# Optimization experiments

Measured on AMD Instinct MI355X. Metric: run time of the kernel, lower is better.

The kernel has to match this reference:

```python
import jax, jax.numpy as jnp
import numpy as np

DIM = 512
HEADS = 8
HEAD_DIM = DIM // HEADS
MLP_HIDDEN = int(DIM * 4.0)
B, N = 4, 2048
LS_INIT = 1e-5
EPS = 1e-5


def _layernorm(x, w, b):
    mu = jnp.mean(x, axis=-1, keepdims=True)
    var = jnp.mean(jnp.square(x - mu), axis=-1, keepdims=True)
    return (x - mu) * jax.lax.rsqrt(var + EPS) * w + b


def setup_inputs() -> dict:
    key = jax.random.key(0)
    ks = jax.random.split(key, 12)
    s = 0.02
    return {
        "x": jax.random.normal(ks[0], (B, N, DIM), jnp.float32),
        "rel_pos_bias": jax.random.normal(ks[1], (HEADS, N, N), jnp.float32),
        "qkv_w": jax.random.normal(ks[2], (DIM, 3 * DIM), jnp.float32) * s,
        "qkv_b": jnp.zeros((3 * DIM,), jnp.float32),
        "out_w": jax.random.normal(ks[3], (DIM, DIM), jnp.float32) * s,
        "out_b": jnp.zeros((DIM,), jnp.float32),
        "ln1_w": jnp.ones((DIM,), jnp.float32),
        "ln1_b": jnp.zeros((DIM,), jnp.float32),
        "ln2_w": jnp.ones((DIM,), jnp.float32),
        "ln2_b": jnp.zeros((DIM,), jnp.float32),
        "ffn_w1": jax.random.normal(ks[4], (DIM, MLP_HIDDEN), jnp.float32) * s,
        "ffn_b1": jnp.zeros((MLP_HIDDEN,), jnp.float32),
        "ffn_w2": jax.random.normal(ks[5], (MLP_HIDDEN, DIM), jnp.float32) * s,
        "ffn_b2": jnp.zeros((DIM,), jnp.float32),
        "gamma1": jnp.full((DIM,), LS_INIT, jnp.float32),
        "gamma2": jnp.full((DIM,), LS_INIT, jnp.float32),
    }


def reference(x, rel_pos_bias, qkv_w, qkv_b, out_w, out_b, ln1_w, ln1_b,
              ln2_w, ln2_b, ffn_w1, ffn_b1, ffn_w2, ffn_b2, gamma1, gamma2):
    # Pre-norm MHA with relative-position bias
    y = _layernorm(x, ln1_w, ln1_b)                       # [B,N,C]
    qkv = y @ qkv_w + qkv_b                               # [B,N,3C]
    qkv = qkv.reshape(B, N, 3, HEADS, HEAD_DIM)
    q = jnp.transpose(qkv[:, :, 0], (0, 2, 1, 3))         # [B,H,N,D]
    k = jnp.transpose(qkv[:, :, 1], (0, 2, 1, 3))
    v = jnp.transpose(qkv[:, :, 2], (0, 2, 1, 3))
    scale = 1.0 / np.sqrt(HEAD_DIM).astype(np.float32)
    attn = jnp.einsum("bhid,bhjd->bhij", q, k) * scale    # [B,H,N,N]
    attn = attn + rel_pos_bias[None]
    attn = jax.nn.softmax(attn, axis=-1)
    out = jnp.einsum("bhij,bhjd->bhid", attn, v)          # [B,H,N,D]
    out = jnp.transpose(out, (0, 2, 1, 3)).reshape(B, N, DIM)
    out = out @ out_w + out_b
    x = x + out * gamma1                                  # layer scale, no drop-path (eval)
    # FFN with exact GELU
    y2 = _layernorm(x, ln2_w, ln2_b)
    h = jax.nn.gelu(y2 @ ffn_w1 + ffn_b1, approximate=False)
    ffn_out = h @ ffn_w2 + ffn_b2
    x = x + ffn_out * gamma2
    return x
```

## Files before the change

kernel.cpp:

```cpp
#include <hip/hip_runtime.h>
#include <hip/hip_bf16.h>
#include <math.h>

#define SEQ 2048
#define BATCH 4
#define DM 512
#define NH 8
#define HD 64
#define HID 2048
#define ROWS (BATCH * SEQ)

typedef __attribute__((ext_vector_type(8))) short short8;
typedef __attribute__((ext_vector_type(4))) float f32x4;

__device__ __forceinline__ short f2bf(float f) {
    unsigned u = __float_as_uint(f);
    u += 0x7fff + ((u >> 16) & 1);
    return (short)(u >> 16);
}

__device__ __forceinline__ void gl2lds16(const void* g, void* l) {
    __builtin_amdgcn_global_load_lds(
        (const __attribute__((address_space(1))) void*)g,
        (__attribute__((address_space(3))) void*)l, 16, 0, 0);
}

__global__ __launch_bounds__(256) void tcast_all(
    const float* __restrict__ qkv_w, const float* __restrict__ out_w,
    const float* __restrict__ w1, const float* __restrict__ w2,
    short* __restrict__ o_qkv, short* __restrict__ o_out,
    short* __restrict__ o_w1, short* __restrict__ o_w2) {
    __shared__ float tile[32][33];
    int id = blockIdx.x;
    const float* W; short* O; int K, N;
    if (id < 768)       { W = qkv_w; O = o_qkv; K = 512;  N = 1536; }
    else if (id < 1024) { W = out_w; O = o_out; K = 512;  N = 512;  id -= 768; }
    else if (id < 2048) { W = w1;    O = o_w1;  K = 512;  N = 2048; id -= 1024; }
    else                { W = w2;    O = o_w2;  K = 2048; N = 512;  id -= 2048; }
    int tn = N / 32;
    int n0 = (id % tn) * 32, k0 = (id / tn) * 32;
    int tx = threadIdx.x, ty = threadIdx.y;
#pragma unroll
    for (int i = 0; i < 4; ++i)
        tile[ty + i * 8][tx] = W[(size_t)(k0 + ty + i * 8) * N + n0 + tx];
    __syncthreads();
#pragma unroll
    for (int i = 0; i < 4; ++i)
        O[(size_t)(n0 + ty + i * 8) * K + k0 + tx] = f2bf(tile[tx][ty + i * 8]);
}

__global__ __launch_bounds__(256) void ln_k(const float* __restrict__ X,
                                            const float* __restrict__ g,
                                            const float* __restrict__ bta,
                                            short* __restrict__ Y) {
    int t = threadIdx.x;
    int wv = t >> 6, ln = t & 63;
    size_t row = (size_t)blockIdx.x * 4 + wv;
    const float* xr = X + row * DM;
    float4 v0 = *(const float4*)(xr + ln * 4);
    float4 v1 = *(const float4*)(xr + 256 + ln * 4);
    float s = v0.x + v0.y + v0.z + v0.w + v1.x + v1.y + v1.z + v1.w;
    float q = v0.x * v0.x + v0.y * v0.y + v0.z * v0.z + v0.w * v0.w +
              v1.x * v1.x + v1.y * v1.y + v1.z * v1.z + v1.w * v1.w;
#pragma unroll
    for (int off = 1; off < 64; off <<= 1) {
        s += __shfl_xor(s, off);
        q += __shfl_xor(q, off);
    }
    float mean = s * (1.0f / 512.0f);
    float var = q * (1.0f / 512.0f) - mean * mean;
    float rstd = rsqrtf(var + 1e-5f);
    int c0 = ln * 4, c1 = 256 + ln * 4;
    ushort4 o0, o1;
    o0.x = (unsigned short)f2bf((v0.x - mean) * rstd * g[c0 + 0] + bta[c0 + 0]);
    o0.y = (unsigned short)f2bf((v0.y - mean) * rstd * g[c0 + 1] + bta[c0 + 1]);
    o0.z = (unsigned short)f2bf((v0.z - mean) * rstd * g[c0 + 2] + bta[c0 + 2]);
    o0.w = (unsigned short)f2bf((v0.w - mean) * rstd * g[c0 + 3] + bta[c0 + 3]);
    o1.x = (unsigned short)f2bf((v1.x - mean) * rstd * g[c1 + 0] + bta[c1 + 0]);
    o1.y = (unsigned short)f2bf((v1.y - mean) * rstd * g[c1 + 1] + bta[c1 + 1]);
    o1.z = (unsigned short)f2bf((v1.z - mean) * rstd * g[c1 + 2] + bta[c1 + 2]);
    o1.w = (unsigned short)f2bf((v1.w - mean) * rstd * g[c1 + 3] + bta[c1 + 3]);
    *(ushort4*)((unsigned short*)Y + row * DM + c0) = o0;
    *(ushort4*)((unsigned short*)Y + row * DM + c1) = o1;
}

template <int EPI, int TN>
__global__ __launch_bounds__(256) void gemm_bt(const short* __restrict__ A,
                                               const short* __restrict__ Bt,
                                               const float* __restrict__ bias,
                                               const float* __restrict__ gamma,
                                               const float* __restrict__ res,
                                               void* __restrict__ Cout,
                                               int M, int N, int K, int gx) {
    constexpr int NI = TN / 32;
    __shared__ __attribute__((aligned(16))) short As[2][2][128][32];
    __shared__ __attribute__((aligned(16))) short Bs[2][2][TN][32];
    int t = threadIdx.x;
    int w = t >> 6, ln = t & 63;
    int quad = ln >> 4, l15 = ln & 15;
    int nwg = gridDim.x;
    int qq = nwg >> 3;
    int sw = ((blockIdx.x & 7) * qq) + (blockIdx.x >> 3);
    int bx = sw % gx, by = sw / gx;
    int n0 = bx * TN, m0 = by * 128;
    int wm = (w & 1) * 64, wn = (w >> 1) * (TN / 2);

    int srow0 = w * 32 + (ln >> 2);
    int srow1 = srow0 + 16;
    int srowB = w * 16 + (ln >> 2);
    int schunk = (ln & 3) * 8;
    const short* Ag0 = A + (size_t)(m0 + srow0) * K + schunk;
    const short* Ag1 = A + (size_t)(m0 + srow1) * K + schunk;
    const short* Bg0 = Bt + (size_t)(n0 + srow0) * K + schunk;
    const short* Bg1 = Bt + (size_t)(n0 + srow1) * K + schunk;
    const short* BgB = Bt + (size_t)(n0 + srowB) * K + schunk;

    f32x4 acc[4][NI];
#pragma unroll
    for (int i = 0; i < 4; ++i)
#pragma unroll
        for (int j = 0; j < NI; ++j) acc[i][j] = (f32x4){0.f, 0.f, 0.f, 0.f};

    auto STAGE = [&](int buf, int k0) {
        gl2lds16(Ag0 + k0, &As[buf][0][srow0][schunk]);
        gl2lds16(Ag1 + k0, &As[buf][0][srow1][schunk]);
        gl2lds16(Ag0 + k0 + 32, &As[buf][1][srow0][schunk]);
        gl2lds16(Ag1 + k0 + 32, &As[buf][1][srow1][schunk]);
        if (TN == 128) {
            gl2lds16(Bg0 + k0, &Bs[buf][0][srow0 & (TN - 1)][schunk]);
            gl2lds16(Bg1 + k0, &Bs[buf][0][srow1 & (TN - 1)][schunk]);
            gl2lds16(Bg0 + k0 + 32, &Bs[buf][1][srow0 & (TN - 1)][schunk]);
            gl2lds16(Bg1 + k0 + 32, &Bs[buf][1][srow1 & (TN - 1)][schunk]);
        } else {
            gl2lds16(BgB + k0, &Bs[buf][0][srowB & (TN - 1)][schunk]);
            gl2lds16(BgB + k0 + 32, &Bs[buf][1][srowB & (TN - 1)][schunk]);
        }
    };

    STAGE(0, 0);
    __syncthreads();

    int NS = K >> 6;
    for (int s = 0; s < NS; ++s) {
        int cur = s & 1;
        if (s + 1 < NS) STAGE(cur ^ 1, (s + 1) << 6);
#pragma unroll
        for (int hh = 0; hh < 2; ++hh) {
            short8 af[4], bf[NI];
#pragma unroll
            for (int mi = 0; mi < 4; ++mi)
                af[mi] = *(const short8*)&As[cur][hh][wm + mi * 16 + l15][quad * 8];
#pragma unroll
            for (int ni = 0; ni < NI; ++ni)
                bf[ni] = *(const short8*)&Bs[cur][hh][wn + ni * 16 + l15][quad * 8];
#pragma unroll
            for (int mi = 0; mi < 4; ++mi)
#pragma unroll
                for (int ni = 0; ni < NI; ++ni)
                    acc[mi][ni] = __builtin_amdgcn_mfma_f32_16x16x32_bf16(
                        af[mi], bf[ni], acc[mi][ni], 0, 0, 0);
        }
        __syncthreads();
    }

#pragma unroll
    for (int mi = 0; mi < 4; ++mi) {
#pragma unroll
        for (int ni = 0; ni < NI; ++ni) {
#pragma unroll
            for (int r = 0; r < 4; ++r) {
                int row = m0 + wm + mi * 16 + quad * 4 + r;
                int col = n0 + wn + ni * 16 + l15;
                float v = acc[mi][ni][r] + bias[col];
                if (EPI == 0) {
                    ((short*)Cout)[(size_t)row * N + col] = f2bf(v);
                } else if (EPI == 1) {
                    float u = v * fmaf(v * v, 0.0713548162f, 1.59576912f);
                    float gg = v / (1.0f + __expf(-u));
                    ((short*)Cout)[(size_t)row * N + col] = f2bf(gg);
                } else {
                    ((float*)Cout)[(size_t)row * N + col] =
                        fmaf(v, gamma[col], res[(size_t)row * N + col]);
                }
            }
        }
    }
}

__global__ __launch_bounds__(256) void qkvbias_k(
    const short* __restrict__ A, const short* __restrict__ Bt,
    const float* __restrict__ qkvb, short* __restrict__ Cout,
    short* __restrict__ Cout2,
    const float* __restrict__ bias, short* __restrict__ biasP) {
    __shared__ __attribute__((aligned(16))) char smem[33024];
    int bid = blockIdx.x;
    int grp = bid / 11, sub = bid % 11;
    int t = threadIdx.x;
    int w = t >> 6, ln = t & 63;
    int quad = ln >> 4, l15 = ln & 15;

    if (sub < 3) {
        typedef short (*tile32)[32];
        tile32 As0 = (tile32)smem;
        tile32 As1 = (tile32)(smem + 8192);
        tile32 Bs0 = (tile32)(smem + 16384);
        tile32 Bs1 = (tile32)(smem + 24576);
        const int K = 512, N = 1536;
        int g = grp * 3 + sub;
        int n0 = (g % 12) * 128, m0 = (g / 12) * 128;
        int wm = (w & 1) * 64, wn = (w >> 1) * 64;

        int srow0 = w * 32 + (ln >> 2);
        int srow1 = srow0 + 16;
        int schunk = (ln & 3) * 8;
        const short* Ag0 = A + (size_t)(m0 + srow0) * K + schunk;
        const short* Ag1 = A + (size_t)(m0 + srow1) * K + schunk;
        const short* Bg0 = Bt + (size_t)(n0 + srow0) * K + schunk;
        const short* Bg1 = Bt + (size_t)(n0 + srow1) * K + schunk;

        f32x4 acc[4][4];
#pragma unroll
        for (int i = 0; i < 4; ++i)
#pragma unroll
            for (int j = 0; j < 4; ++j) acc[i][j] = (f32x4){0.f, 0.f, 0.f, 0.f};

        for (int k0 = 0; k0 < K; k0 += 64) {
            __syncthreads();
            gl2lds16(Ag0 + k0, &As0[srow0][schunk]);
            gl2lds16(Ag1 + k0, &As0[srow1][schunk]);
            gl2lds16(Ag0 + k0 + 32, &As1[srow0][schunk]);
            gl2lds16(Ag1 + k0 + 32, &As1[srow1][schunk]);
            gl2lds16(Bg0 + k0, &Bs0[srow0][schunk]);
            gl2lds16(Bg1 + k0, &Bs0[srow1][schunk]);
            gl2lds16(Bg0 + k0 + 32, &Bs1[srow0][schunk]);
            gl2lds16(Bg1 + k0 + 32, &Bs1[srow1][schunk]);
            __syncthreads();
            {
                short8 af[4], bf[4];
#pragma unroll
                for (int mi = 0; mi < 4; ++mi)
                    af[mi] = *(const short8*)&As0[wm + mi * 16 + l15][quad * 8];
#pragma unroll
                for (int ni = 0; ni < 4; ++ni)
                    bf[ni] = *(const short8*)&Bs0[wn + ni * 16 + l15][quad * 8];
#pragma unroll
                for (int mi = 0; mi < 4; ++mi)
#pragma unroll
                    for (int ni = 0; ni < 4; ++ni)
                        acc[mi][ni] = __builtin_amdgcn_mfma_f32_16x16x32_bf16(
                            af[mi], bf[ni], acc[mi][ni], 0, 0, 0);
            }
            {
                short8 af[4], bf[4];
#pragma unroll
                for (int mi = 0; mi < 4; ++mi)
                    af[mi] = *(const short8*)&As1[wm + mi * 16 + l15][quad * 8];
#pragma unroll
                for (int ni = 0; ni < 4; ++ni)
                    bf[ni] = *(const short8*)&Bs1[wn + ni * 16 + l15][quad * 8];
#pragma unroll
                for (int mi = 0; mi < 4; ++mi)
#pragma unroll
                    for (int ni = 0; ni < 4; ++ni)
                        acc[mi][ni] = __builtin_amdgcn_mfma_f32_16x16x32_bf16(
                            af[mi], bf[ni], acc[mi][ni], 0, 0, 0);
            }
        }

        if (n0 >= 1024) {
#pragma unroll
            for (int mi = 0; mi < 4; ++mi) {
#pragma unroll
                for (int ni = 0; ni < 4; ++ni) {
                    int col = n0 + wn + ni * 16 + l15;
                    int d = col - 1024, hh = d >> 6, dd = d & 63;
                    int row0 = m0 + wm + mi * 16 + quad * 4;
                    int bb = row0 >> 11, key = row0 & 2047;
                    float bs = qkvb[col];
                    ushort4 pk;
                    pk.x = (unsigned short)f2bf(acc[mi][ni][0] + bs);
                    pk.y = (unsigned short)f2bf(acc[mi][ni][1] + bs);
                    pk.z = (unsigned short)f2bf(acc[mi][ni][2] + bs);
                    pk.w = (unsigned short)f2bf(acc[mi][ni][3] + bs);
                    *(ushort4*)&Cout2[((size_t)(bb * 8 + hh) * 64 + dd) * 2048 + key] = pk;
                }
            }
        } else {
#pragma unroll
            for (int mi = 0; mi < 4; ++mi) {
#pragma unroll
                for (int ni = 0; ni < 4; ++ni) {
#pragma unroll
                    for (int r = 0; r < 4; ++r) {
                        int row = m0 + wm + mi * 16 + quad * 4 + r;
                        int col = n0 + wn + ni * 16 + l15;
                        float v = acc[mi][ni][r] + qkvb[col];
                        float sc = (n0 < 512) ? 0.18033688f : 1.0f;
                        Cout[(size_t)row * 1024 + col] = f2bf(v * sc);
                    }
                }
            }
        }
    } else {
        typedef short (*tile1032)[1032];
        tile1032 tl = (tile1032)smem;
        int id = grp * 8 + (sub - 3);
        int half = id & 1;
        int g = (id >> 1) & 127;
        int h = id >> 8;
        const float* src = bias + (size_t)h * SEQ * SEQ + (size_t)g * 16 * SEQ + half * 1024;
#pragma unroll
        for (int i = 0; i < 16; ++i) {
            float4 v = *(const float4*)(src + (size_t)i * SEQ + t * 4);
            float2 lo, hi;
            lo.x = v.x * 1.44269504f; lo.y = v.y * 1.44269504f;
            hi.x = v.z * 1.44269504f; hi.y = v.w * 1.44269504f;
            __hip_bfloat162 l2 = __float22bfloat162_rn(lo);
            __hip_bfloat162 h2 = __float22bfloat162_rn(hi);
            uint2 pp;
            pp.x = *(unsigned*)&l2;
            pp.y = *(unsigned*)&h2;
            *(uint2*)&tl[i][t * 4] = pp;
        }
        __syncthreads();
        int jtbase = half * 16;
#pragma unroll
        for (int u = 0; u < 4; ++u) {
            int jl = w * 4 + u;
            int tau = (h * 128 + g) * 32 + jtbase + jl;
#pragma unroll
            for (int n2 = 0; n2 < 2; ++n2) {
                uint2 a = *(const uint2*)&tl[l15][jl * 64 + n2 * 32 + quad * 4];
                uint2 b = *(const uint2*)&tl[l15][jl * 64 + n2 * 32 + 16 + quad * 4];
                uint4 pp;
                pp.x = a.x; pp.y = a.y; pp.z = b.x; pp.w = b.y;
                *(uint4*)(biasP + (size_t)tau * 1024 + n2 * 512 + ln * 8) = pp;
            }
        }
    }
}

__global__ __launch_bounds__(256, 3) void attn_k(const short* __restrict__ qkv,
                                                 const short* __restrict__ vT,
                                                 const short* __restrict__ biasP,
                                                 short* __restrict__ Aout) {
    __shared__ __attribute__((aligned(16))) short Ks[2][64 * 64];
    __shared__ __attribute__((aligned(16))) short Vs[2][64 * 64];
    __shared__ __attribute__((aligned(16))) short Ps[4][2][16 * 64];
    int t = threadIdx.x;
    int w = t >> 6, ln = t & 63, quad = ln >> 4, l15 = ln & 15;
    int idx = blockIdx.x;
    int h = idx & 7, b = (idx >> 3) & 3, qt = idx >> 5;
    int qb = qt * 128 + w * 16;
    const size_t cbase = (size_t)b * SEQ * 1024;

    const short* qrow0 = qkv + cbase + (size_t)(qb + l15) * 1024 + h * 64;
    const short* qrow1 = qrow0 + (size_t)64 * 1024;
    short8 qf[2][2];
    qf[0][0] = *(const short8*)(qrow0 + quad * 8);
    qf[0][1] = *(const short8*)(qrow0 + 32 + quad * 8);
    qf[1][0] = *(const short8*)(qrow1 + quad * 8);
    qf[1][1] = *(const short8*)(qrow1 + 32 + quad * 8);

    int kr = t >> 3, kc = t & 7;
    int sc = (kc ^ (kr & 7)) * 8;
    const short* kgS = qkv + cbase + 512 + h * 64 + sc;
    const short* vgS = vT + (size_t)(b * 8 + h) * 64 * 2048 + sc;

    int g0 = qt * 8 + w;
    const short* bp0 = biasP + ((size_t)(h * 128 + g0) * 32) * 1024 + ln * 8;
    const short* bp1 = biasP + ((size_t)(h * 128 + g0 + 4) * 32) * 1024 + ln * 8;

    short8 ones;
#pragma unroll
    for (int i = 0; i < 8; ++i) ones[i] = (short)0x3F80;

    f32x4 o[2][4], ol[2];
#pragma unroll
    for (int qg = 0; qg < 2; ++qg) {
#pragma unroll
        for (int db = 0; db < 4; ++db) o[qg][db] = (f32x4){0.f, 0.f, 0.f, 0.f};
        ol[qg] = (f32x4){0.f, 0.f, 0.f, 0.f};
    }

    int sw7 = l15 & 7;

    gl2lds16(kgS,                              &Ks[0][t * 8]);
    gl2lds16(kgS + (size_t)32 * 1024,          &Ks[0][2048 + t * 8]);
    gl2lds16(vgS,                              &Vs[0][t * 8]);
    gl2lds16(vgS + (size_t)32 * 2048,          &Vs[0][2048 + t * 8]);
    uint4 bbc[2][2];
#pragma unroll
    for (int n2 = 0; n2 < 2; ++n2) {
        bbc[0][n2] = *(const uint4*)(bp0 + n2 * 512);
        bbc[1][n2] = *(const uint4*)(bp1 + n2 * 512);
    }

    int cur = 0;
    for (int jt = 0; jt < 32; ++jt) {
        __syncthreads();
        int jn = (jt < 31) ? (jt + 1) : jt;
        int j1 = jn * 64;
        int nxt = cur ^ 1;
        gl2lds16(kgS + (size_t)(j1 + kr) * 1024,      &Ks[nxt][t * 8]);
        gl2lds16(kgS + (size_t)(j1 + 32 + kr) * 1024, &Ks[nxt][2048 + t * 8]);
        gl2lds16(vgS + (size_t)kr * 2048 + j1,        &Vs[nxt][t * 8]);
        gl2lds16(vgS + (size_t)(32 + kr) * 2048 + j1, &Vs[nxt][2048 + t * 8]);

        f32x4 s4[2][4];
#pragma unroll
        for (int ni = 0; ni < 4; ++ni) {
            short8 k0 = *(const short8*)&Ks[cur][(ni * 16 + l15) * 64 + ((quad ^ sw7) * 8)];
            short8 k1 = *(const short8*)&Ks[cur][(ni * 16 + l15) * 64 + (((4 + quad) ^ sw7) * 8)];
#pragma unroll
            for (int qg = 0; qg < 2; ++qg) {
                uint4 bb = bbc[qg][ni >> 1];
                unsigned lo = (ni & 1) ? bb.z : bb.x;
                unsigned hi = (ni & 1) ? bb.w : bb.y;
                f32x4 z;
                z[0] = __uint_as_float(lo << 16);
                z[1] = __uint_as_float(lo & 0xffff0000u);
                z[2] = __uint_as_float(hi << 16);
                z[3] = __uint_as_float(hi & 0xffff0000u);
                z = __builtin_amdgcn_mfma_f32_16x16x32_bf16(k0, qf[qg][0], z, 0, 0, 0);
                s4[qg][ni] = __builtin_amdgcn_mfma_f32_16x16x32_bf16(k1, qf[qg][1], z, 0, 0, 0);
            }
        }
#pragma unroll
        for (int n2 = 0; n2 < 2; ++n2) {
            bbc[0][n2] = *(const uint4*)(bp0 + (size_t)jn * 1024 + n2 * 512);
            bbc[1][n2] = *(const uint4*)(bp1 + (size_t)jn * 1024 + n2 * 512);
        }
#pragma unroll
        for (int qg = 0; qg < 2; ++qg) {
#pragma unroll
            for (int ni = 0; ni < 4; ++ni) {
                float2 plo, phi;
                plo.x = exp2f(s4[qg][ni][0]);
                plo.y = exp2f(s4[qg][ni][1]);
                phi.x = exp2f(s4[qg][ni][2]);
                phi.y = exp2f(s4[qg][ni][3]);
                __hip_bfloat162 l2 = __float22bfloat162_rn(plo);
                __hip_bfloat162 h2 = __float22bfloat162_rn(phi);
                union { uint2 u; } pp;
                pp.u.x = *(unsigned*)&l2;
                pp.u.y = *(unsigned*)&h2;
                int c = ni * 2 + (quad >> 1);
                *(uint2*)&Ps[w][qg][l15 * 64 + ((c ^ sw7) * 8) + (quad & 1) * 4] = pp.u;
            }
        }
#pragma unroll
        for (int kk = 0; kk < 2; ++kk) {
            short8 ap0 = *(const short8*)&Ps[w][0][l15 * 64 + (((kk * 4 + quad) ^ sw7) * 8)];
            short8 ap1 = *(const short8*)&Ps[w][1][l15 * 64 + (((kk * 4 + quad) ^ sw7) * 8)];
#pragma unroll
            for (int db = 0; db < 4; ++db) {
                short8 vv = *(const short8*)&Vs[cur][(db * 16 + l15) * 64 + (((kk * 4 + quad) ^ sw7) * 8)];
                o[0][db] = __builtin_amdgcn_mfma_f32_16x16x32_bf16(ap0, vv, o[0][db], 0, 0, 0);
                o[1][db] = __builtin_amdgcn_mfma_f32_16x16x32_bf16(ap1, vv, o[1][db], 0, 0, 0);
            }
            ol[0] = __builtin_amdgcn_mfma_f32_16x16x32_bf16(ap0, ones, ol[0], 0, 0, 0);
            ol[1] = __builtin_amdgcn_mfma_f32_16x16x32_bf16(ap1, ones, ol[1], 0, 0, 0);
        }
        cur = nxt;
    }
#pragma unroll
    for (int qg = 0; qg < 2; ++qg) {
#pragma unroll
        for (int r = 0; r < 4; ++r) {
            float inv = 1.0f / ol[qg][r];
            int qrow_g = b * SEQ + qb + qg * 64 + quad * 4 + r;
#pragma unroll
            for (int db = 0; db < 4; ++db) {
                Aout[(size_t)qrow_g * DM + h * 64 + db * 16 + l15] =
                    f2bf(o[qg][db][r] * inv);
            }
        }
    }
}

extern "C" void kernel_launch(void* const* d_in, const int* in_sizes, int n_in,
                              void* d_out, int out_size, void* d_ws, size_t ws_size,
                              hipStream_t stream) {
    const float* x      = (const float*)d_in[0];
    const float* bias   = (const float*)d_in[1];
    const float* qkv_w  = (const float*)d_in[2];
    const float* qkv_b  = (const float*)d_in[3];
    const float* out_w  = (const float*)d_in[4];
    const float* out_b  = (const float*)d_in[5];
    const float* ln1_w  = (const float*)d_in[6];
    const float* ln1_b  = (const float*)d_in[7];
    const float* ln2_w  = (const float*)d_in[8];
    const float* ln2_b  = (const float*)d_in[9];
    const float* ffn_w1 = (const float*)d_in[10];
    const float* ffn_b1 = (const float*)d_in[11];
    const float* ffn_w2 = (const float*)d_in[12];
    const float* ffn_b2 = (const float*)d_in[13];
    const float* gamma1 = (const float*)d_in[14];
    const float* gamma2 = (const float*)d_in[15];
    float* out = (float*)d_out;

    short* wqkvT = (short*)d_ws;
    short* woutT = wqkvT + (size_t)1536 * 512;
    short* w1T   = woutT + (size_t)512 * 512;
    short* w2T   = w1T + (size_t)2048 * 512;
    short* y1    = w2T + (size_t)512 * 2048;
    short* qkvB  = y1 + (size_t)ROWS * DM;
    short* vTb   = qkvB + (size_t)ROWS * 1024;
    short* aoutB = vTb + (size_t)32 * 64 * 2048;
    float* x1    = (float*)(aoutB + (size_t)ROWS * DM);
    short* biasPw = (short*)(x1 + (size_t)ROWS * DM);
    short* hB    = qkvB;

    tcast_all<<<3072, dim3(32, 8), 0, stream>>>(qkv_w, out_w, ffn_w1, ffn_w2,
                                                wqkvT, woutT, w1T, w2T);
    ln_k<<<ROWS / 4, 256, 0, stream>>>(x, ln1_w, ln1_b, y1);
    qkvbias_k<<<2816, 256, 0, stream>>>(y1, wqkvT, qkv_b, qkvB, vTb,
                                        bias, biasPw);
    attn_k<<<512, 256, 0, stream>>>(qkvB, vTb, biasPw, aoutB);
    gemm_bt<2, 128><<<256, 256, 0, stream>>>(
        aoutB, woutT, out_b, gamma1, x, x1, ROWS, 512, 512, 4);
    ln_k<<<ROWS / 4, 256, 0, stream>>>(x1, ln2_w, ln2_b, y1);
    gemm_bt<1, 128><<<1024, 256, 0, stream>>>(
        y1, w1T, ffn_b1, nullptr, nullptr, hB, ROWS, 2048, 512, 16);
    gemm_bt<2, 128><<<256, 256, 0, stream>>>(
        hB, w2T, ffn_b2, gamma2, x1, out, ROWS, 512, 2048, 4);
}
```

Before: 431.4 us.

## Split attention KV range into two halves with separate combine kernel

Each attention block now handles only half of the key/value tiles, so the grid doubles from 512 to 1024 blocks. Each half writes unnormalized fp32 partial outputs and row sums to workspace. A new combine kernel adds the two partials, divides by the total row sum and writes the bf16 attention output. This is meant to fill more of the GPU's compute units and block slots. The cost is extra fp32 partial-output traffic, one more kernel launch, and more workspace, part of which reuses the x1 buffer.

New measurement: 444.9 us. 1.03x slower.

```diff
diff --git a/kernel.cpp b/kernel.cpp
--- a/kernel.cpp
+++ b/kernel.cpp
@@ -343,15 +343,21 @@
 __global__ __launch_bounds__(256, 3) void attn_k(const short* __restrict__ qkv,
                                                  const short* __restrict__ vT,
                                                  const short* __restrict__ biasP,
-                                                 short* __restrict__ Aout) {
+                                                 float* __restrict__ O0,
+                                                 float* __restrict__ O1,
+                                                 float* __restrict__ lp) {
     __shared__ __attribute__((aligned(16))) short Ks[2][64 * 64];
     __shared__ __attribute__((aligned(16))) short Vs[2][64 * 64];
     __shared__ __attribute__((aligned(16))) short Ps[4][2][16 * 64];
     int t = threadIdx.x;
     int w = t >> 6, ln = t & 63, quad = ln >> 4, l15 = ln & 15;
     int idx = blockIdx.x;
-    int h = idx & 7, b = (idx >> 3) & 3, qt = idx >> 5;
+    int half = idx >> 9;
+    int rest = idx & 511;
+    int h = rest & 7, b = (rest >> 3) & 3, qt = rest >> 5;
     int qb = qt * 128 + w * 16;
+    int jt0 = half * 16;
+    int j0 = jt0 * 64;
     const size_t cbase = (size_t)b * SEQ * 1024;
 
     const short* qrow0 = qkv + cbase + (size_t)(qb + l15) * 1024 + h * 64;
@@ -385,21 +391,21 @@
 
     int sw7 = l15 & 7;
 
-    gl2lds16(kgS,                              &Ks[0][t * 8]);
-    gl2lds16(kgS + (size_t)32 * 1024,          &Ks[0][2048 + t * 8]);
-    gl2lds16(vgS,                              &Vs[0][t * 8]);
-    gl2lds16(vgS + (size_t)32 * 2048,          &Vs[0][2048 + t * 8]);
+    gl2lds16(kgS + (size_t)(j0 + kr) * 1024,      &Ks[0][t * 8]);
+    gl2lds16(kgS + (size_t)(j0 + 32 + kr) * 1024, &Ks[0][2048 + t * 8]);
+    gl2lds16(vgS + (size_t)kr * 2048 + j0,        &Vs[0][t * 8]);
+    gl2lds16(vgS + (size_t)(32 + kr) * 2048 + j0, &Vs[0][2048 + t * 8]);
     uint4 bbc[2][2];
 #pragma unroll
     for (int n2 = 0; n2 < 2; ++n2) {
-        bbc[0][n2] = *(const uint4*)(bp0 + n2 * 512);
-        bbc[1][n2] = *(const uint4*)(bp1 + n2 * 512);
+        bbc[0][n2] = *(const uint4*)(bp0 + (size_t)jt0 * 1024 + n2 * 512);
+        bbc[1][n2] = *(const uint4*)(bp1 + (size_t)jt0 * 1024 + n2 * 512);
     }
 
     int cur = 0;
-    for (int jt = 0; jt < 32; ++jt) {
+    for (int jt = jt0; jt < jt0 + 16; ++jt) {
         __syncthreads();
-        int jn = (jt < 31) ? (jt + 1) : jt;
+        int jn = (jt < jt0 + 15) ? (jt + 1) : jt;
         int j1 = jn * 64;
         int nxt = cur ^ 1;
         gl2lds16(kgS + (size_t)(j1 + kr) * 1024,      &Ks[nxt][t * 8]);
@@ -464,19 +470,52 @@
         }
         cur = nxt;
     }
+    float* Od = half ? O1 : O0;
+    float* ld = lp + half * (32 * 2048);
 #pragma unroll
     for (int qg = 0; qg < 2; ++qg) {
 #pragma unroll
         for (int r = 0; r < 4; ++r) {
-            float inv = 1.0f / ol[qg][r];
-            int qrow_g = b * SEQ + qb + qg * 64 + quad * 4 + r;
+            int qloc = qb + qg * 64 + quad * 4 + r;
+            int qrow_g = b * SEQ + qloc;
 #pragma unroll
             for (int db = 0; db < 4; ++db) {
-                Aout[(size_t)qrow_g * DM + h * 64 + db * 16 + l15] =
-                    f2bf(o[qg][db][r] * inv);
-            }
-        }
-    }
+                Od[(size_t)qrow_g * DM + h * 64 + db * 16 + l15] = o[qg][db][r];
+            }
+            if (l15 == 0)
+                ld[(size_t)(b * 8 + h) * 2048 + qloc] = ol[qg][r];
+        }
+    }
+}
+
+__global__ __launch_bounds__(256) void comb_k(const float* __restrict__ O0,
+                                              const float* __restrict__ O1,
+                                              const float* __restrict__ lp,
+                                              short* __restrict__ Aout) {
+    int t = threadIdx.x;
+    int wv = t >> 6, ln = t & 63;
+    size_t row = (size_t)blockIdx.x * 4 + wv;
+    int b = (int)(row >> 11), q = (int)(row & 2047);
+    int h = ln >> 3;
+    float la = lp[(size_t)(b * 8 + h) * 2048 + q];
+    float lb = lp[32 * 2048 + (size_t)(b * 8 + h) * 2048 + q];
+    float inv = 1.0f / (la + lb);
+    const float* p0 = O0 + row * DM + ln * 8;
+    const float* p1 = O1 + row * DM + ln * 8;
+    float4 a0 = *(const float4*)p0;
+    float4 a1 = *(const float4*)(p0 + 4);
+    float4 c0 = *(const float4*)p1;
+    float4 c1 = *(const float4*)(p1 + 4);
+    short8 o;
+    o[0] = f2bf((a0.x + c0.x) * inv);
+    o[1] = f2bf((a0.y + c0.y) * inv);
+    o[2] = f2bf((a0.z + c0.z) * inv);
+    o[3] = f2bf((a0.w + c0.w) * inv);
+    o[4] = f2bf((a1.x + c1.x) * inv);
+    o[5] = f2bf((a1.y + c1.y) * inv);
+    o[6] = f2bf((a1.z + c1.z) * inv);
+    o[7] = f2bf((a1.w + c1.w) * inv);
+    *(short8*)(Aout + row * DM + ln * 8) = o;
 }
 
 extern "C" void kernel_launch(void* const* d_in, const int* in_sizes, int n_in,
@@ -510,6 +549,9 @@
     short* aoutB = vTb + (size_t)32 * 64 * 2048;
     float* x1    = (float*)(aoutB + (size_t)ROWS * DM);
     short* biasPw = (short*)(x1 + (size_t)ROWS * DM);
+    float* opart1 = (float*)(biasPw + (size_t)8 * 2048 * 2048);
+    float* lpart  = opart1 + (size_t)ROWS * DM;
+    float* opart0 = x1;
     short* hB    = qkvB;
 
     tcast_all<<<3072, dim3(32, 8), 0, stream>>>(qkv_w, out_w, ffn_w1, ffn_w2,
@@ -517,7 +559,8 @@
     ln_k<<<ROWS / 4, 256, 0, stream>>>(x, ln1_w, ln1_b, y1);
     qkvbias_k<<<2816, 256, 0, stream>>>(y1, wqkvT, qkv_b, qkvB, vTb,
                                         bias, biasPw);
-    attn_k<<<512, 256, 0, stream>>>(qkvB, vTb, biasPw, aoutB);
+    attn_k<<<1024, 256, 0, stream>>>(qkvB, vTb, biasPw, opart0, opart1, lpart);
+    comb_k<<<ROWS / 4, 256, 0, stream>>>(opart0, opart1, lpart, aoutB);
     gemm_bt<2, 128><<<256, 256, 0, stream>>>(
         aoutB, woutT, out_b, gamma1, x, x1, ROWS, 512, 512, 4);
     ln_k<<<ROWS / 4, 256, 0, stream>>>(x1, ln2_w, ln2_b, y1);
```
